# Performance work log

Measured on AMD Instinct MI355X. Metric: run time of the kernel, lower is better.

Reference implementation:

```python
import jax, jax.numpy as jnp
import numpy as np

TEMPERATURE = 0.07
BASE_TEMPERATURE = 0.07


def setup_inputs() -> dict:
    key = jax.random.key(0)
    k1, k2 = jax.random.split(key)
    N, D = 8192, 512
    features = jax.random.normal(k1, (N, D), dtype=jnp.float32)
    labels = jax.random.randint(k2, (N,), 0, 64, dtype=jnp.int64 if jax.config.jax_enable_x64 else jnp.int32)
    return {"features": features, "labels": labels, "rotation_multiplier": 2}


def reference(features, labels, rotation_multiplier):
    k = int(rotation_multiplier)
    N = features.shape[0]
    B = N // k
    # L2-normalize rows (torch F.normalize clamps norm at eps=1e-12)
    norm = jnp.maximum(jnp.linalg.norm(features, axis=1, keepdims=True), 1e-12)
    f = features / norm
    sim = jnp.matmul(f, f.T) / TEMPERATURE  # [N, N]

    # block positive mask: groups of k rows share a label; compare group labels
    lab = labels.reshape(B, k)[:, 0]  # [B]
    same = lab[:, None] == lab[None, :]  # [B, B]
    mask = jnp.repeat(jnp.repeat(same, k, axis=0), k, axis=1)  # [N, N]
    eye = jnp.eye(N, dtype=bool)
    mask = mask & ~eye

    # stable masked log-softmax with diagonal removed from denominator
    logits_max = jax.lax.stop_gradient(jnp.max(sim, axis=1, keepdims=True))
    logits = sim - logits_max
    exp_logits = jnp.exp(logits)
    denom = exp_logits.sum(axis=1, keepdims=True) - jnp.diagonal(exp_logits)[:, None] + 1e-8
    log_prob = logits - jnp.log(denom)

    mask_f = mask.astype(logits.dtype)
    mask_sum = mask_f.sum(axis=1)  # [N]
    valid = mask_sum > 0
    mean_log_prob_pos = (log_prob * mask_f).sum(axis=1) / jnp.maximum(mask_sum, 1.0)
    per_sample = -(TEMPERATURE / BASE_TEMPERATURE) * mean_log_prob_pos
    n_valid = valid.sum().astype(logits.dtype)
    loss = jnp.where(valid, per_sample, 0.0).sum() / jnp.maximum(n_valid, 1.0)
    return loss
```

## Files before the change

kernel.cpp:

```cpp
#include <hip/hip_runtime.h>
#include <hip/hip_bf16.h>

#define TEMP_INV 14.285714285714286f
#define FSCALE 16.0f
#define T1S (TEMP_INV / 256.0f)

typedef __attribute__((ext_vector_type(4))) float f32x4;
typedef __attribute__((ext_vector_type(4))) int i32x4;
typedef __attribute__((ext_vector_type(8))) int i32x8;


__global__ __launch_bounds__(256) void norm_k(const float* __restrict__ feat,
                                              uchar* __restrict__ fq,
                                              const int* __restrict__ labels,
                                              const int* __restrict__ kptr,
                                              int* __restrict__ glab,
                                              float* __restrict__ gacc,
                                              int* __restrict__ dcnt,
                                              int N, int D) {
  const int row = (blockIdx.x * 256 + threadIdx.x) >> 6;
  const int lane = threadIdx.x & 63;
  if (row < N) {
    const float4* fr = (const float4*)(feat + (size_t)row * D);
    float4 v0 = fr[lane * 2];
    float4 v1 = fr[lane * 2 + 1];
    float ss = v0.x * v0.x + v0.y * v0.y + v0.z * v0.z + v0.w * v0.w +
               v1.x * v1.x + v1.y * v1.y + v1.z * v1.z + v1.w * v1.w;
    #pragma unroll
    for (int off = 32; off; off >>= 1) ss += __shfl_xor(ss, off, 64);
    const float inv = FSCALE / fmaxf(sqrtf(ss), 1e-12f);
    int w0 = 0, w1 = 0;
    w0 = __builtin_amdgcn_cvt_pk_fp8_f32(v0.x * inv, v0.y * inv, w0, false);
    w0 = __builtin_amdgcn_cvt_pk_fp8_f32(v0.z * inv, v0.w * inv, w0, true);
    w1 = __builtin_amdgcn_cvt_pk_fp8_f32(v1.x * inv, v1.y * inv, w1, false);
    w1 = __builtin_amdgcn_cvt_pk_fp8_f32(v1.z * inv, v1.w * inv, w1, true);
    uint2 o; o.x = (uint)w0; o.y = (uint)w1;
    const int tkb  = lane >> 4;
    const int quad = (lane >> 2) & 3;
    const int half = (lane >> 1) & 1;
    const int slot = half * 64 + quad * 16 + (row & 15);
    uchar* dstp = fq + (((size_t)(row >> 4) * (D >> 7) + tkb) << 11) +
                  slot * 16 + (lane & 1) * 8;
    *(uint2*)dstp = o;
    if (lane == 0) {
      const int k = *kptr;
      glab[row] = labels[(size_t)(row / k) * k];
    }
  }
  if (blockIdx.x == 0 && threadIdx.x < 3) {
    if (threadIdx.x < 2) gacc[threadIdx.x] = 0.f;
    else *dcnt = 0;
  }
}

__global__ __launch_bounds__(64) void gemm_k(const uchar* __restrict__ fq,
                                             const int* __restrict__ glab,
                                             float* __restrict__ part,
                                             int N, int D) {
  const int lane = threadIdx.x;
  const int quad = lane >> 4, l15 = lane & 15;

  const int nbs = N / 64;
  const int total = nbs * (nbs + 1) / 2;
  int gidx = blockIdx.x;
  if ((total & 7) == 0) {
    const int per = total >> 3;
    gidx = (blockIdx.x & 7) * per + (blockIdx.x >> 3);
  }
  const float nf = (float)nbs + 0.5f;
  int bi = (int)(nf - sqrtf(fmaxf(nf * nf - 2.0f * (float)gidx, 0.f)));
  if (bi < 0) bi = 0;
  if (bi > nbs - 1) bi = nbs - 1;
  while (bi > 0 && bi * nbs - bi * (bi - 1) / 2 > gidx) bi--;
  while ((bi + 1) * nbs - (bi + 1) * bi / 2 <= gidx) bi++;
  const int bj = bi + (gidx - (bi * nbs - bi * (bi - 1) / 2));
  const int i0 = bi * 64, j0 = bj * 64;
  const bool diagblk = (bi == bj);

  f32x4 acc[4][4];
  #pragma unroll
  for (int mi = 0; mi < 4; mi++)
    #pragma unroll
    for (int ni = 0; ni < 4; ni++) {
      f32x4 z = {0.f, 0.f, 0.f, 0.f};
      acc[mi][ni] = z;
    }

  const int ktiles = D >> 7;
  const uchar* ap = fq + (((size_t)(i0 >> 4) * ktiles) << 11) + lane * 16;
  const uchar* bp = fq + (((size_t)(j0 >> 4) * ktiles) << 11) + lane * 16;

#define KSTEP(kt)                                                             \
  {                                                                           \
    i32x8 bv[4];                                                              \
    _Pragma("unroll")                                                         \
    for (int ni = 0; ni < 4; ni++) {                                          \
      const uchar* p = bp + (((ni) * ktiles + (kt)) << 11);                   \
      i32x4 lo = *(const i32x4*)p;                                            \
      i32x4 hi = *(const i32x4*)(p + 1024);                                   \
      bv[ni] = (i32x8){lo.x, lo.y, lo.z, lo.w, hi.x, hi.y, hi.z, hi.w};       \
    }                                                                         \
    _Pragma("unroll")                                                         \
    for (int mi = 0; mi < 4; mi++) {                                          \
      const uchar* p = ap + (((mi) * ktiles + (kt)) << 11);                   \
      i32x4 lo = *(const i32x4*)p;                                            \
      i32x4 hi = *(const i32x4*)(p + 1024);                                   \
      i32x8 av = (i32x8){lo.x, lo.y, lo.z, lo.w, hi.x, hi.y, hi.z, hi.w};     \
      _Pragma("unroll")                                                       \
      for (int ni = 0; ni < 4; ni++)                                          \
        acc[mi][ni] = __builtin_amdgcn_mfma_scale_f32_16x16x128_f8f6f4(       \
            av, bv[ni], acc[mi][ni], 0, 0, 0, 127, 0, 127);                   \
    }                                                                         \
  }

  if (ktiles == 4) {
    KSTEP(0) KSTEP(1) KSTEP(2) KSTEP(3)
  } else {
    for (int kt = 0; kt < ktiles; kt++) KSTEP(kt)
  }
#undef KSTEP

  int clab[4];
  #pragma unroll
  for (int ni = 0; ni < 4; ni++) clab[ni] = glab[j0 + ni * 16 + l15];

  float colE[4] = {0.f, 0.f, 0.f, 0.f};
  float colP[4] = {0.f, 0.f, 0.f, 0.f};
  float* dst = part + (size_t)gidx * 256;

  #pragma unroll
  for (int mi = 0; mi < 4; mi++) {
    const int lrw = mi * 16 + quad * 4;
    #pragma unroll
    for (int r = 0; r < 4; r++) {
      const int row = i0 + lrw + r;
      const int rlab = glab[row];
      float Ssum = 0.f, Psum = 0.f;
      #pragma unroll
      for (int ni = 0; ni < 4; ni++) {
        const int col = j0 + ni * 16 + l15;
        const float val = acc[mi][ni][r];
        const float lg = fmaf(val, T1S, -TEMP_INV);
        const bool diag = diagblk && (row == col);
        const float e = diag ? 0.f : __expf(lg);
        const float pm = (!diag && rlab == clab[ni]) ? lg : 0.f;
        Ssum += e; Psum += pm;
        colE[ni] += e; colP[ni] += pm;
      }
      #pragma unroll
      for (int off = 8; off; off >>= 1) {
        Ssum += __shfl_xor(Ssum, off, 64);
        Psum += __shfl_xor(Psum, off, 64);
      }
      if (l15 == 0) {
        dst[lrw + r]      = Ssum;
        dst[64 + lrw + r] = Psum;
      }
    }
  }
  if (!diagblk) {
    #pragma unroll
    for (int ni = 0; ni < 4; ni++) {
      float e = colE[ni];
      float p = colP[ni];
      e += __shfl_xor(e, 16, 64);
      e += __shfl_xor(e, 32, 64);
      p += __shfl_xor(p, 16, 64);
      p += __shfl_xor(p, 32, 64);
      if (quad == 0) {
        dst[128 + ni * 16 + l15] = e;
        dst[192 + ni * 16 + l15] = p;
      }
    }
  }
}

__global__ __launch_bounds__(1024) void reduce_loss_k(const float* __restrict__ part,
                                                      const int* __restrict__ glab,
                                                      const int* __restrict__ labels,
                                                      const int* __restrict__ kptr,
                                                      float* __restrict__ gacc,
                                                      int* __restrict__ dcnt,
                                                      float* __restrict__ out, int N) {
  const int nbs = N / 64;
  const int b = blockIdx.x;
  const int tt = threadIdx.x;
  const int t = tt & 63;
  const int sl = tt >> 6;
  const int k = *kptr;
  const int B = N / k;

  __shared__ int h[64];
  if (tt < 64) h[tt] = 0;
  __syncthreads();
  for (int g = tt; g < B; g += 1024) {
    int lb = labels[(size_t)g * k];
    if (lb >= 0 && lb < 64) atomicAdd(&h[lb], 1);
  }

  float S = 0.f, P = 0.f;
  const int base = b * nbs - b * (b - 1) / 2;
  for (int bj = b + sl; bj < nbs; bj += 16) {
    const float* p = part + (size_t)(base + bj - b) * 256;
    S += p[t];
    P += p[64 + t];
  }
  for (int bi = sl; bi < b; bi += 16) {
    const int idx = bi * nbs - bi * (bi - 1) / 2 + (b - bi);
    const float* p = part + (size_t)idx * 256;
    S += p[128 + t];
    P += p[192 + t];
  }
  __shared__ float sS[16][64], sP[16][64];
  sS[sl][t] = S; sP[sl][t] = P;
  __syncthreads();
  float l = 0.f, v = 0.f;
  if (sl == 0) {
    S = 0.f; P = 0.f;
    #pragma unroll
    for (int s = 0; s < 16; s++) { S += sS[s][t]; P += sP[s][t]; }
    const int np = h[glab[b * 64 + t]] * k - 1;
    if (np > 0) {
      l = -(P - (float)np * logf(S + 1e-8f)) / (float)np;
      v = 1.f;
    }
  }
  #pragma unroll
  for (int off = 32; off; off >>= 1) {
    l += __shfl_xor(l, off, 64);
    v += __shfl_xor(v, off, 64);
  }
  __shared__ float sl16[16], sv16[16];
  if ((tt & 63) == 0) { sl16[tt >> 6] = l; sv16[tt >> 6] = v; }
  __syncthreads();
  if (tt == 0) {
    float L = 0.f, V = 0.f;
    #pragma unroll
    for (int i = 0; i < 16; i++) { L += sl16[i]; V += sv16[i]; }
    atomicAdd(&gacc[0], L);
    atomicAdd(&gacc[1], V);
    __threadfence();
    const int prev = atomicAdd(dcnt, 1);
    if (prev == (int)gridDim.x - 1) {
      const float Lf = atomicAdd(&gacc[0], 0.f);
      const float Vf = atomicAdd(&gacc[1], 0.f);
      out[0] = Lf / fmaxf(Vf, 1.f);
    }
  }
}

extern "C" void kernel_launch(void* const* d_in, const int* in_sizes, int n_in,
                              void* d_out, int out_size, void* d_ws, size_t ws_size,
                              hipStream_t stream) {
  const float* feat = (const float*)d_in[0];
  const int* labels = (const int*)d_in[1];
  const int* kptr   = (const int*)d_in[2];
  const int N = in_sizes[1];
  const int D = in_sizes[0] / N;

  const int nbs = N / 64;
  const int total = nbs * (nbs + 1) / 2;

  char* ws = (char*)d_ws;
  uchar* fq = (uchar*)ws;
  size_t off = (size_t)N * D;
  float* part = (float*)(ws + off); off += (size_t)total * 256 * sizeof(float);
  int* glab   = (int*)(ws + off);   off += (size_t)N * sizeof(int);
  float* gacc = (float*)(ws + off); off += 2 * sizeof(float);
  int* dcnt   = (int*)(ws + off);   off += sizeof(int);

  norm_k<<<(N + 3) / 4, 256, 0, stream>>>(feat, fq, labels, kptr, glab,
                                          gacc, dcnt, N, D);
  gemm_k<<<total, 64, 0, stream>>>(fq, glab, part, N, D);
  reduce_loss_k<<<nbs, 1024, 0, stream>>>(part, glab, labels, kptr, gacc, dcnt,
                                          (float*)d_out, N);
}
```

Measured before the change: 133.6 us.

## Replace symmetric triangle tiling with full row-strip sweep and per-slice row partials

The GEMM kernel no longer exploits symmetry of the similarity matrix. Each wave now owns a 32-row strip with A fragments held in registers and sweeps one of eight column slices, accumulating row sums of exp and positive logits in registers. Partials shrink to eight per row, and the reduce kernel becomes a simple per-row sum. This removes column-partial bookkeeping and the triangular index math, but doubles the MFMA and exponential work and lowers reuse of each loaded B tile.

```diff
diff --git a/kernel.cpp b/kernel.cpp
--- a/kernel.cpp
+++ b/kernel.cpp
@@ -53,173 +53,191 @@
   }
 }
 
-__global__ __launch_bounds__(64) void gemm_k(const uchar* __restrict__ fq,
-                                             const int* __restrict__ glab,
-                                             float* __restrict__ part,
-                                             int N, int D) {
-  const int lane = threadIdx.x;
+__global__ __launch_bounds__(128) void gemm_k(const uchar* __restrict__ fq,
+                                              const int* __restrict__ glab,
+                                              float* __restrict__ partS,
+                                              float* __restrict__ partP,
+                                              int N, int D) {
+  const int lane = threadIdx.x & 63;
+  const int wid  = threadIdx.x >> 6;
   const int quad = lane >> 4, l15 = lane & 15;
-
-  const int nbs = N / 64;
-  const int total = nbs * (nbs + 1) / 2;
-  int gidx = blockIdx.x;
-  if ((total & 7) == 0) {
-    const int per = total >> 3;
-    gidx = (blockIdx.x & 7) * per + (blockIdx.x >> 3);
-  }
-  const float nf = (float)nbs + 0.5f;
-  int bi = (int)(nf - sqrtf(fmaxf(nf * nf - 2.0f * (float)gidx, 0.f)));
-  if (bi < 0) bi = 0;
-  if (bi > nbs - 1) bi = nbs - 1;
-  while (bi > 0 && bi * nbs - bi * (bi - 1) / 2 > gidx) bi--;
-  while ((bi + 1) * nbs - (bi + 1) * bi / 2 <= gidx) bi++;
-  const int bj = bi + (gidx - (bi * nbs - bi * (bi - 1) / 2));
-  const int i0 = bi * 64, j0 = bj * 64;
-  const bool diagblk = (bi == bj);
-
-  f32x4 acc[4][4];
+  const int ktiles = D >> 7;
+  const int strip = (blockIdx.x >> 3) * 2 + wid;
+  const int slice = blockIdx.x & 7;
+  const int r0 = strip * 32;
+  const int cps = N >> 3;
+  const int jsteps = cps >> 6;
+  const int j0base = slice * cps;
+
+  int rlab[2][4];
   #pragma unroll
-  for (int mi = 0; mi < 4; mi++)
-    #pragma unroll
-    for (int ni = 0; ni < 4; ni++) {
-      f32x4 z = {0.f, 0.f, 0.f, 0.f};
-      acc[mi][ni] = z;
-    }
-
-  const int ktiles = D >> 7;
-  const uchar* ap = fq + (((size_t)(i0 >> 4) * ktiles) << 11) + lane * 16;
-  const uchar* bp = fq + (((size_t)(j0 >> 4) * ktiles) << 11) + lane * 16;
-
-#define KSTEP(kt)                                                             \
+  for (int mi = 0; mi < 2; mi++)
+    #pragma unroll
+    for (int r = 0; r < 4; r++)
+      rlab[mi][r] = glab[r0 + mi * 16 + quad * 4 + r];
+
+  float Srun[2][4] = {{0.f, 0.f, 0.f, 0.f}, {0.f, 0.f, 0.f, 0.f}};
+  float Prun[2][4] = {{0.f, 0.f, 0.f, 0.f}, {0.f, 0.f, 0.f, 0.f}};
+
+#define LOADF(dst, grp, kt)                                                   \
   {                                                                           \
-    i32x8 bv[4];                                                              \
-    _Pragma("unroll")                                                         \
-    for (int ni = 0; ni < 4; ni++) {                                          \
-      const uchar* p = bp + (((ni) * ktiles + (kt)) << 11);                   \
-      i32x4 lo = *(const i32x4*)p;                                            \
-      i32x4 hi = *(const i32x4*)(p + 1024);                                   \
-      bv[ni] = (i32x8){lo.x, lo.y, lo.z, lo.w, hi.x, hi.y, hi.z, hi.w};       \
-    }                                                                         \
-    _Pragma("unroll")                                                         \
-    for (int mi = 0; mi < 4; mi++) {                                          \
-      const uchar* p = ap + (((mi) * ktiles + (kt)) << 11);                   \
-      i32x4 lo = *(const i32x4*)p;                                            \
-      i32x4 hi = *(const i32x4*)(p + 1024);                                   \
-      i32x8 av = (i32x8){lo.x, lo.y, lo.z, lo.w, hi.x, hi.y, hi.z, hi.w};     \
-      _Pragma("unroll")                                                       \
-      for (int ni = 0; ni < 4; ni++)                                          \
-        acc[mi][ni] = __builtin_amdgcn_mfma_scale_f32_16x16x128_f8f6f4(       \
-            av, bv[ni], acc[mi][ni], 0, 0, 0, 127, 0, 127);                   \
-    }                                                                         \
+    const uchar* p_ = fq + (((size_t)((grp) * ktiles + (kt))) << 11) + lane * 16; \
+    i32x4 lo_ = *(const i32x4*)p_;                                            \
+    i32x4 hi_ = *(const i32x4*)(p_ + 1024);                                   \
+    dst = (i32x8){lo_.x, lo_.y, lo_.z, lo_.w, hi_.x, hi_.y, hi_.z, hi_.w};    \
   }
 
   if (ktiles == 4) {
-    KSTEP(0) KSTEP(1) KSTEP(2) KSTEP(3)
+    i32x8 af[2][4];
+    #pragma unroll
+    for (int mi = 0; mi < 2; mi++)
+      #pragma unroll
+      for (int kt = 0; kt < 4; kt++)
+        LOADF(af[mi][kt], (r0 >> 4) + mi, kt)
+
+    for (int js = 0; js < jsteps; js++) {
+      const int j0 = j0base + js * 64;
+      f32x4 acc[2][4];
+      #pragma unroll
+      for (int mi = 0; mi < 2; mi++)
+        #pragma unroll
+        for (int ni = 0; ni < 4; ni++) {
+          f32x4 z = {0.f, 0.f, 0.f, 0.f};
+          acc[mi][ni] = z;
+        }
+      #pragma unroll
+      for (int kt = 0; kt < 4; kt++) {
+        i32x8 bv[4];
+        #pragma unroll
+        for (int ni = 0; ni < 4; ni++)
+          LOADF(bv[ni], (j0 >> 4) + ni, kt)
+        #pragma unroll
+        for (int mi = 0; mi < 2; mi++)
+          #pragma unroll
+          for (int ni = 0; ni < 4; ni++)
+            acc[mi][ni] = __builtin_amdgcn_mfma_scale_f32_16x16x128_f8f6f4(
+                af[mi][kt], bv[ni], acc[mi][ni], 0, 0, 0, 127, 0, 127);
+      }
+      int clab[4];
+      #pragma unroll
+      for (int ni = 0; ni < 4; ni++) clab[ni] = glab[j0 + ni * 16 + l15];
+      #pragma unroll
+      for (int mi = 0; mi < 2; mi++)
+        #pragma unroll
+        for (int r = 0; r < 4; r++) {
+          const int row = r0 + mi * 16 + quad * 4 + r;
+          const int rl = rlab[mi][r];
+          float s = 0.f, pp = 0.f;
+          #pragma unroll
+          for (int ni = 0; ni < 4; ni++) {
+            const int col = j0 + ni * 16 + l15;
+            const float lg = fmaf(acc[mi][ni][r], T1S, -TEMP_INV);
+            const bool diag = (col == row);
+            s += diag ? 0.f : __expf(lg);
+            pp += (!diag && rl == clab[ni]) ? lg : 0.f;
+          }
+          Srun[mi][r] += s;
+          Prun[mi][r] += pp;
+        }
+    }
   } else {
-    for (int kt = 0; kt < ktiles; kt++) KSTEP(kt)
-  }
-#undef KSTEP
-
-  int clab[4];
+    for (int js = 0; js < jsteps; js++) {
+      const int j0 = j0base + js * 64;
+      f32x4 acc[2][4];
+      #pragma unroll
+      for (int mi = 0; mi < 2; mi++)
+        #pragma unroll
+        for (int ni = 0; ni < 4; ni++) {
+          f32x4 z = {0.f, 0.f, 0.f, 0.f};
+          acc[mi][ni] = z;
+        }
+      for (int kt = 0; kt < ktiles; kt++) {
+        i32x8 as[2], bv[4];
+        #pragma unroll
+        for (int mi = 0; mi < 2; mi++) LOADF(as[mi], (r0 >> 4) + mi, kt)
+        #pragma unroll
+        for (int ni = 0; ni < 4; ni++) LOADF(bv[ni], (j0 >> 4) + ni, kt)
+        #pragma unroll
+        for (int mi = 0; mi < 2; mi++)
+          #pragma unroll
+          for (int ni = 0; ni < 4; ni++)
+            acc[mi][ni] = __builtin_amdgcn_mfma_scale_f32_16x16x128_f8f6f4(
+                as[mi], bv[ni], acc[mi][ni], 0, 0, 0, 127, 0, 127);
+      }
+      int clab[4];
+      #pragma unroll
+      for (int ni = 0; ni < 4; ni++) clab[ni] = glab[j0 + ni * 16 + l15];
+      #pragma unroll
+      for (int mi = 0; mi < 2; mi++)
+        #pragma unroll
+        for (int r = 0; r < 4; r++) {
+          const int row = r0 + mi * 16 + quad * 4 + r;
+          const int rl = rlab[mi][r];
+          float s = 0.f, pp = 0.f;
+          #pragma unroll
+          for (int ni = 0; ni < 4; ni++) {
+            const int col = j0 + ni * 16 + l15;
+            const float lg = fmaf(acc[mi][ni][r], T1S, -TEMP_INV);
+            const bool diag = (col == row);
+            s += diag ? 0.f : __expf(lg);
+            pp += (!diag && rl == clab[ni]) ? lg : 0.f;
+          }
+          Srun[mi][r] += s;
+          Prun[mi][r] += pp;
+        }
+    }
+  }
+#undef LOADF
+
   #pragma unroll
-  for (int ni = 0; ni < 4; ni++) clab[ni] = glab[j0 + ni * 16 + l15];
-
-  float colE[4] = {0.f, 0.f, 0.f, 0.f};
-  float colP[4] = {0.f, 0.f, 0.f, 0.f};
-  float* dst = part + (size_t)gidx * 256;
-
-  #pragma unroll
-  for (int mi = 0; mi < 4; mi++) {
-    const int lrw = mi * 16 + quad * 4;
+  for (int mi = 0; mi < 2; mi++)
     #pragma unroll
     for (int r = 0; r < 4; r++) {
-      const int row = i0 + lrw + r;
-      const int rlab = glab[row];
-      float Ssum = 0.f, Psum = 0.f;
-      #pragma unroll
-      for (int ni = 0; ni < 4; ni++) {
-        const int col = j0 + ni * 16 + l15;
-        const float val = acc[mi][ni][r];
-        const float lg = fmaf(val, T1S, -TEMP_INV);
-        const bool diag = diagblk && (row == col);
-        const float e = diag ? 0.f : __expf(lg);
-        const float pm = (!diag && rlab == clab[ni]) ? lg : 0.f;
-        Ssum += e; Psum += pm;
-        colE[ni] += e; colP[ni] += pm;
-      }
-      #pragma unroll
-      for (int off = 8; off; off >>= 1) {
-        Ssum += __shfl_xor(Ssum, off, 64);
-        Psum += __shfl_xor(Psum, off, 64);
+      float s = Srun[mi][r], p = Prun[mi][r];
+      #pragma unroll
+      for (int off = 1; off < 16; off <<= 1) {
+        s += __shfl_xor(s, off, 64);
+        p += __shfl_xor(p, off, 64);
       }
       if (l15 == 0) {
-        dst[lrw + r]      = Ssum;
-        dst[64 + lrw + r] = Psum;
-      }
-    }
-  }
-  if (!diagblk) {
-    #pragma unroll
-    for (int ni = 0; ni < 4; ni++) {
-      float e = colE[ni];
-      float p = colP[ni];
-      e += __shfl_xor(e, 16, 64);
-      e += __shfl_xor(e, 32, 64);
-      p += __shfl_xor(p, 16, 64);
-      p += __shfl_xor(p, 32, 64);
-      if (quad == 0) {
-        dst[128 + ni * 16 + l15] = e;
-        dst[192 + ni * 16 + l15] = p;
-      }
-    }
-  }
-}
-
-__global__ __launch_bounds__(1024) void reduce_loss_k(const float* __restrict__ part,
-                                                      const int* __restrict__ glab,
-                                                      const int* __restrict__ labels,
-                                                      const int* __restrict__ kptr,
-                                                      float* __restrict__ gacc,
-                                                      int* __restrict__ dcnt,
-                                                      float* __restrict__ out, int N) {
-  const int nbs = N / 64;
-  const int b = blockIdx.x;
+        const int row = r0 + mi * 16 + quad * 4 + r;
+        partS[(size_t)row * 8 + slice] = s;
+        partP[(size_t)row * 8 + slice] = p;
+      }
+    }
+}
+
+__global__ __launch_bounds__(256) void reduce_loss_k(const float* __restrict__ partS,
+                                                     const float* __restrict__ partP,
+                                                     const int* __restrict__ glab,
+                                                     const int* __restrict__ labels,
+                                                     const int* __restrict__ kptr,
+                                                     float* __restrict__ gacc,
+                                                     int* __restrict__ dcnt,
+                                                     float* __restrict__ out, int N) {
   const int tt = threadIdx.x;
-  const int t = tt & 63;
-  const int sl = tt >> 6;
+  const int row = blockIdx.x * 256 + tt;
   const int k = *kptr;
   const int B = N / k;
 
   __shared__ int h[64];
   if (tt < 64) h[tt] = 0;
   __syncthreads();
-  for (int g = tt; g < B; g += 1024) {
+  for (int g = tt; g < B; g += 256) {
     int lb = labels[(size_t)g * k];
     if (lb >= 0 && lb < 64) atomicAdd(&h[lb], 1);
   }
-
-  float S = 0.f, P = 0.f;
-  const int base = b * nbs - b * (b - 1) / 2;
-  for (int bj = b + sl; bj < nbs; bj += 16) {
-    const float* p = part + (size_t)(base + bj - b) * 256;
-    S += p[t];
-    P += p[64 + t];
-  }
-  for (int bi = sl; bi < b; bi += 16) {
-    const int idx = bi * nbs - bi * (bi - 1) / 2 + (b - bi);
-    const float* p = part + (size_t)idx * 256;
-    S += p[128 + t];
-    P += p[192 + t];
-  }
-  __shared__ float sS[16][64], sP[16][64];
-  sS[sl][t] = S; sP[sl][t] = P;
   __syncthreads();
+
   float l = 0.f, v = 0.f;
-  if (sl == 0) {
-    S = 0.f; P = 0.f;
-    #pragma unroll
-    for (int s = 0; s < 16; s++) { S += sS[s][t]; P += sP[s][t]; }
-    const int np = h[glab[b * 64 + t]] * k - 1;
+  if (row < N) {
+    float S = 0.f, P = 0.f;
+    #pragma unroll
+    for (int s = 0; s < 8; s++) {
+      S += partS[(size_t)row * 8 + s];
+      P += partP[(size_t)row * 8 + s];
+    }
+    const int np = h[glab[row]] * k - 1;
     if (np > 0) {
       l = -(P - (float)np * logf(S + 1e-8f)) / (float)np;
       v = 1.f;
@@ -230,13 +248,13 @@
     l += __shfl_xor(l, off, 64);
     v += __shfl_xor(v, off, 64);
   }
-  __shared__ float sl16[16], sv16[16];
-  if ((tt & 63) == 0) { sl16[tt >> 6] = l; sv16[tt >> 6] = v; }
+  __shared__ float sl4[4], sv4[4];
+  if ((tt & 63) == 0) { sl4[tt >> 6] = l; sv4[tt >> 6] = v; }
   __syncthreads();
   if (tt == 0) {
     float L = 0.f, V = 0.f;
     #pragma unroll
-    for (int i = 0; i < 16; i++) { L += sl16[i]; V += sv16[i]; }
+    for (int i = 0; i < 4; i++) { L += sl4[i]; V += sv4[i]; }
     atomicAdd(&gacc[0], L);
     atomicAdd(&gacc[1], V);
     __threadfence();
@@ -258,20 +276,22 @@
   const int N = in_sizes[1];
   const int D = in_sizes[0] / N;
 
-  const int nbs = N / 64;
-  const int total = nbs * (nbs + 1) / 2;
-
   char* ws = (char*)d_ws;
   uchar* fq = (uchar*)ws;
   size_t off = (size_t)N * D;
-  float* part = (float*)(ws + off); off += (size_t)total * 256 * sizeof(float);
-  int* glab   = (int*)(ws + off);   off += (size_t)N * sizeof(int);
-  float* gacc = (float*)(ws + off); off += 2 * sizeof(float);
-  int* dcnt   = (int*)(ws + off);   off += sizeof(int);
+  float* partS = (float*)(ws + off); off += (size_t)N * 8 * sizeof(float);
+  float* partP = (float*)(ws + off); off += (size_t)N * 8 * sizeof(float);
+  int* glab    = (int*)(ws + off);   off += (size_t)N * sizeof(int);
+  float* gacc  = (float*)(ws + off); off += 2 * sizeof(float);
+  int* dcnt    = (int*)(ws + off);   off += sizeof(int);
+
+  const int strips = N / 32;
+  const int ggrid = (strips / 2) * 8;
 
   norm_k<<<(N + 3) / 4, 256, 0, stream>>>(feat, fq, labels, kptr, glab,
                                           gacc, dcnt, N, D);
-  gemm_k<<<total, 64, 0, stream>>>(fq, glab, part, N, D);
-  reduce_loss_k<<<nbs, 1024, 0, stream>>>(part, glab, labels, kptr, gacc, dcnt,
-                                          (float*)d_out, N);
-}
+  gemm_k<<<ggrid, 128, 0, stream>>>(fq, glab, partS, partP, N, D);
+  reduce_loss_k<<<(N + 255) / 256, 256, 0, stream>>>(partS, partP, glab, labels,
+                                                     kptr, gacc, dcnt,
+                                                     (float*)d_out, N);
+}
```

New measurement: 125.6 us, median of 2. 1.06x faster.
